# Kernel tuning notes

Measured on AMD Instinct MI355X. Metric: run time of the kernel, lower is better.

The kernel has to match this reference:

```python
import jax, jax.numpy as jnp
import numpy as np

N_REAL = 1_000_000
C_IN = 32
C_OUT = 32
PAD = 1_050_000


def setup_inputs() -> dict:
    key = jax.random.key(0)
    k_x, k_fn, k_w0, k_w1, k_w2, k_b = jax.random.split(key, 6)
    x = jax.random.normal(k_x, (N_REAL, C_IN), dtype=jnp.float32)
    face_neighborhood = jax.random.randint(k_fn, (N_REAL, 9), 0, PAD, dtype=jnp.int32)
    # real faces occupy the first N_REAL padded slots; the rest are pads
    face_is_pad = jnp.arange(PAD) >= N_REAL
    # kaiming-uniform-style init for [out, in] weights (fan_in = C_IN for 1x1 taps)
    bw = 1.0 / np.sqrt(C_IN)
    w0 = jax.random.uniform(k_w0, (C_OUT, C_IN), jnp.float32, -bw, bw)
    w1 = jax.random.uniform(k_w1, (C_OUT, C_IN), jnp.float32, -bw, bw)
    w2 = jax.random.uniform(k_w2, (C_OUT, C_IN), jnp.float32, -bw, bw)
    bb = 1.0 / np.sqrt(C_IN * 9)  # fan_in of the full (out,in,1,9) kernel
    bias = jax.random.uniform(k_b, (C_OUT,), jnp.float32, -bb, bb)
    return {"x": x, "w0": w0, "w1": w1, "w2": w2, "bias": bias,
            "face_neighborhood": face_neighborhood, "face_is_pad": face_is_pad,
            "pad_size": PAD}


def reference(x, w0, w1, w2, bias, face_neighborhood, face_is_pad, pad_size):
    # Scatter x into padded buffer: padded_x[~face_is_pad] = x (jit-safe via cumsum map)
    keep = jnp.logical_not(face_is_pad)
    src = jnp.cumsum(keep.astype(jnp.int32)) - 1  # index into x for each kept slot
    padded_x = jnp.where(keep[:, None], x[jnp.clip(src, 0, x.shape[0] - 1)],
                         jnp.zeros((), x.dtype))  # [pad_size, C]
    # Symmetric 1x9 filter = [w0, w1, w2, w1, w2, w1, w2, w1, w2]:
    # fold the 9 gathers into 3 groups before the tiny GEMMs.
    g0 = padded_x[face_neighborhood[:, 0]]
    g1 = (padded_x[face_neighborhood[:, 1]] + padded_x[face_neighborhood[:, 3]]
          + padded_x[face_neighborhood[:, 5]] + padded_x[face_neighborhood[:, 7]])
    g2 = (padded_x[face_neighborhood[:, 2]] + padded_x[face_neighborhood[:, 4]]
          + padded_x[face_neighborhood[:, 6]] + padded_x[face_neighborhood[:, 8]])
    out = (jnp.einsum('nc,oc->no', g0, w0)
           + jnp.einsum('nc,oc->no', g1, w1)
           + jnp.einsum('nc,oc->no', g2, w2)
           + bias)
    return out
```

## Files before the change

### kernel.cpp

```cpp
#include <hip/hip_runtime.h>
#include <hip/hip_fp16.h>

typedef _Float16 half8 __attribute__((ext_vector_type(8)));
typedef _Float16 half4v __attribute__((ext_vector_type(4)));
typedef float float4v __attribute__((ext_vector_type(4)));

#define BLOCK 256
#define ROWS_PER_BLOCK 64
#define ROWPITCH 104

__device__ _Float16 g_wh[6 * 512];

__global__ void prep_weights(const float* __restrict__ w0,
                             const float* __restrict__ w1,
                             const float* __restrict__ w2) {
    const int t = threadIdx.x;
    const int st = t >> 6;
    const int lane = t & 63;
    const int s = st >> 1, tt = st & 1;
    const float* w = (s == 0) ? w0 : (s == 1) ? w1 : w2;
    const int o = tt * 16 + (lane & 15);
    const int k = (lane >> 4) * 8;
    #pragma unroll
    for (int j = 0; j < 8; ++j)
        g_wh[st * 512 + lane * 8 + j] = (_Float16)w[o * 32 + k + j];
}

__global__ __launch_bounds__(BLOCK) void face_conv_kernel(
    const float* __restrict__ x,
    const float* __restrict__ bias,
    const int* __restrict__ fn,
    float* __restrict__ out,
    int N)
{
    __shared__ _Float16 A[4][16 * ROWPITCH];

    const int tid  = threadIdx.x;
    const int wave = tid >> 6;
    const int lane = tid & 63;
    const int m16  = lane & 15;
    const int quad = lane >> 4;
    const int oct  = lane >> 3;
    const int m8   = lane & 7;

    half8 bfrag[3][2];
    #pragma unroll
    for (int s = 0; s < 3; ++s)
        #pragma unroll
        for (int t = 0; t < 2; ++t)
            bfrag[s][t] = *(const half8*)(g_wh + (s * 2 + t) * 512 + lane * 8);
    const float bias0 = bias[m16];
    const float bias1 = bias[16 + m16];

    const int base = blockIdx.x * ROWS_PER_BLOCK + wave * 16;
    _Float16* Aw = A[wave];

    int idx[2][9];
    #pragma unroll
    for (int it = 0; it < 2; ++it) {
        int r = base + it * 8 + oct;
        r = (r < N) ? r : (N - 1);
        const int* fr = fn + (long)r * 9;
        #pragma unroll
        for (int j = 0; j < 9; ++j) idx[it][j] = __builtin_nontemporal_load(fr + j);
    }

    #pragma unroll
    for (int it = 0; it < 2; ++it) {
        float4v v[9];
        #pragma unroll
        for (int j = 0; j < 9; ++j) {
            const int id = idx[it][j];
            if ((unsigned)id < (unsigned)N) {
                v[j] = *(const float4v*)(x + (long)id * 32 + m8 * 4);
            } else {
                v[j] = (float4v){0.f, 0.f, 0.f, 0.f};
            }
        }
        const float4v g0 = v[0];
        const float4v g1 = v[1] + v[3] + v[5] + v[7];
        const float4v g2 = v[2] + v[4] + v[6] + v[8];
        _Float16* dst = Aw + (it * 8 + oct) * ROWPITCH + m8 * 4;
        *(half4v*)(dst)      = (half4v){(_Float16)g0.x, (_Float16)g0.y, (_Float16)g0.z, (_Float16)g0.w};
        *(half4v*)(dst + 32) = (half4v){(_Float16)g1.x, (_Float16)g1.y, (_Float16)g1.z, (_Float16)g1.w};
        *(half4v*)(dst + 64) = (half4v){(_Float16)g2.x, (_Float16)g2.y, (_Float16)g2.z, (_Float16)g2.w};
    }

    __syncthreads();

    float4v acc0 = {0.f, 0.f, 0.f, 0.f}, acc1 = {0.f, 0.f, 0.f, 0.f};
    #pragma unroll
    for (int s = 0; s < 3; ++s) {
        half8 a = *(half8*)(Aw + m16 * ROWPITCH + s * 32 + quad * 8);
        acc0 = __builtin_amdgcn_mfma_f32_16x16x32_f16(a, bfrag[s][0], acc0, 0, 0, 0);
        acc1 = __builtin_amdgcn_mfma_f32_16x16x32_f16(a, bfrag[s][1], acc1, 0, 0, 0);
    }

    #pragma unroll
    for (int i = 0; i < 4; ++i) {
        const int r = base + quad * 4 + i;
        if (r < N) {
            __builtin_nontemporal_store(acc0[i] + bias0, &out[(long)r * 32 + m16]);
            __builtin_nontemporal_store(acc1[i] + bias1, &out[(long)r * 32 + 16 + m16]);
        }
    }
}

extern "C" void kernel_launch(void* const* d_in, const int* in_sizes, int n_in,
                              void* d_out, int out_size, void* d_ws, size_t ws_size,
                              hipStream_t stream) {
    const float* x    = (const float*)d_in[0];
    const float* w0   = (const float*)d_in[1];
    const float* w1   = (const float*)d_in[2];
    const float* w2   = (const float*)d_in[3];
    const float* bias = (const float*)d_in[4];
    const int*   fn   = (const int*)d_in[5];
    float* out = (float*)d_out;

    const int N = in_sizes[0] / 32;
    const int blocks = (N + ROWS_PER_BLOCK - 1) / ROWS_PER_BLOCK;

    prep_weights<<<1, 384, 0, stream>>>(w0, w1, w2);
    face_conv_kernel<<<blocks, BLOCK, 0, stream>>>(x, bias, fn, out, N);
}
```

Baseline: 378.4 us.

## Pre-convert x to fp16 in workspace and gather half-precision rows

Adds a pass that converts x to fp16 into the workspace buffer. A new conv kernel then gathers 16-byte half8 chunks, so each random gather moves half the bytes, and neighbor indices are loaded as int4 vectors. The cost is an extra streaming read of x plus a write of the fp16 copy. The values are also rounded to fp16 before the group sums, where before they were summed in fp32 first. The fp32 path remains as a fallback when the workspace is too small.

After: 401.6 us. +6.1%, slower.

```diff
diff --git a/kernel.cpp b/kernel.cpp
--- a/kernel.cpp
+++ b/kernel.cpp
@@ -4,6 +4,7 @@
 typedef _Float16 half8 __attribute__((ext_vector_type(8)));
 typedef _Float16 half4v __attribute__((ext_vector_type(4)));
 typedef float float4v __attribute__((ext_vector_type(4)));
+typedef int int4a __attribute__((ext_vector_type(4), aligned(4)));
 
 #define BLOCK 256
 #define ROWS_PER_BLOCK 64
@@ -26,6 +27,97 @@
         g_wh[st * 512 + lane * 8 + j] = (_Float16)w[o * 32 + k + j];
 }
 
+__global__ __launch_bounds__(256) void convert_x(const float* __restrict__ x,
+                                                 _Float16* __restrict__ xh,
+                                                 int n8) {
+    const int stride = gridDim.x * 256;
+    for (int i = blockIdx.x * 256 + threadIdx.x; i < n8; i += stride) {
+        const float4v a = __builtin_nontemporal_load(reinterpret_cast<const float4v*>(x) + 2 * (long)i);
+        const float4v b = __builtin_nontemporal_load(reinterpret_cast<const float4v*>(x) + 2 * (long)i + 1);
+        half8 h = {(_Float16)a.x, (_Float16)a.y, (_Float16)a.z, (_Float16)a.w,
+                   (_Float16)b.x, (_Float16)b.y, (_Float16)b.z, (_Float16)b.w};
+        *(half8*)(xh + 8 * (long)i) = h;
+    }
+}
+
+__global__ __launch_bounds__(BLOCK) void face_conv_f16(
+    const _Float16* __restrict__ xh,
+    const float* __restrict__ bias,
+    const int* __restrict__ fn,
+    float* __restrict__ out,
+    int N)
+{
+    __shared__ alignas(16) _Float16 A[4][16 * ROWPITCH];
+
+    const int tid  = threadIdx.x;
+    const int wave = tid >> 6;
+    const int lane = tid & 63;
+    const int m16  = lane & 15;
+    const int quad = lane >> 4;
+    const int r    = lane >> 2;
+    const int c8   = (lane & 3) * 8;
+
+    half8 bfrag[3][2];
+    #pragma unroll
+    for (int s = 0; s < 3; ++s)
+        #pragma unroll
+        for (int t = 0; t < 2; ++t)
+            bfrag[s][t] = *(const half8*)(g_wh + (s * 2 + t) * 512 + lane * 8);
+    const float bias0 = bias[m16];
+    const float bias1 = bias[16 + m16];
+
+    const int base = blockIdx.x * ROWS_PER_BLOCK + wave * 16;
+    _Float16* Aw = A[wave];
+
+    int row = base + r;
+    row = (row < N) ? row : (N - 1);
+    const int* fr = fn + (long)row * 9;
+    const int4a i03 = __builtin_nontemporal_load(reinterpret_cast<const int4a*>(fr));
+    const int4a i47 = __builtin_nontemporal_load(reinterpret_cast<const int4a*>(fr + 4));
+    const int  i8s  = __builtin_nontemporal_load(fr + 8);
+    const int idx[9] = {i03.x, i03.y, i03.z, i03.w, i47.x, i47.y, i47.z, i47.w, i8s};
+
+    half8 v[9];
+    #pragma unroll
+    for (int j = 0; j < 9; ++j) {
+        const int id = idx[j];
+        if ((unsigned)id < (unsigned)N) {
+            v[j] = *(const half8*)(xh + (long)id * 32 + c8);
+        } else {
+            v[j] = (half8){0, 0, 0, 0, 0, 0, 0, 0};
+        }
+    }
+    half8 g0 = v[0], g1, g2;
+    #pragma unroll
+    for (int e = 0; e < 8; ++e) {
+        g1[e] = (_Float16)((float)v[1][e] + (float)v[3][e] + (float)v[5][e] + (float)v[7][e]);
+        g2[e] = (_Float16)((float)v[2][e] + (float)v[4][e] + (float)v[6][e] + (float)v[8][e]);
+    }
+    _Float16* dst = Aw + r * ROWPITCH + c8;
+    *(half8*)(dst)      = g0;
+    *(half8*)(dst + 32) = g1;
+    *(half8*)(dst + 64) = g2;
+
+    __syncthreads();
+
+    float4v acc0 = {0.f, 0.f, 0.f, 0.f}, acc1 = {0.f, 0.f, 0.f, 0.f};
+    #pragma unroll
+    for (int s = 0; s < 3; ++s) {
+        half8 a = *(half8*)(Aw + m16 * ROWPITCH + s * 32 + quad * 8);
+        acc0 = __builtin_amdgcn_mfma_f32_16x16x32_f16(a, bfrag[s][0], acc0, 0, 0, 0);
+        acc1 = __builtin_amdgcn_mfma_f32_16x16x32_f16(a, bfrag[s][1], acc1, 0, 0, 0);
+    }
+
+    #pragma unroll
+    for (int i = 0; i < 4; ++i) {
+        const int rr = base + quad * 4 + i;
+        if (rr < N) {
+            __builtin_nontemporal_store(acc0[i] + bias0, &out[(long)rr * 32 + m16]);
+            __builtin_nontemporal_store(acc1[i] + bias1, &out[(long)rr * 32 + 16 + m16]);
+        }
+    }
+}
+
 __global__ __launch_bounds__(BLOCK) void face_conv_kernel(
     const float* __restrict__ x,
     const float* __restrict__ bias,
@@ -33,7 +125,7 @@
     float* __restrict__ out,
     int N)
 {
-    __shared__ _Float16 A[4][16 * ROWPITCH];
+    __shared__ alignas(16) _Float16 A[4][16 * ROWPITCH];
 
     const int tid  = threadIdx.x;
     const int wave = tid >> 6;
@@ -121,5 +213,14 @@
     const int blocks = (N + ROWS_PER_BLOCK - 1) / ROWS_PER_BLOCK;
 
     prep_weights<<<1, 384, 0, stream>>>(w0, w1, w2);
-    face_conv_kernel<<<blocks, BLOCK, 0, stream>>>(x, bias, fn, out, N);
-}
+
+    const size_t need = (size_t)N * 32 * sizeof(_Float16);
+    if (d_ws != nullptr && ws_size >= need) {
+        _Float16* xh = (_Float16*)d_ws;
+        const int n8 = N * 4;
+        convert_x<<<2048, 256, 0, stream>>>(x, xh, n8);
+        face_conv_f16<<<blocks, BLOCK, 0, stream>>>(xh, bias, fn, out, N);
+    } else {
+        face_conv_kernel<<<blocks, BLOCK, 0, stream>>>(x, bias, fn, out, N);
+    }
+}
```

## Issue all 18 gather loads upfront with 4 lanes per row and vectorized index loads

Applied to the files above, without the earlier changes.

Each lane now owns a quarter-row (8 floats), so every row is gathered by 4 lanes, and all 18 float4 gathers are issued at once with branchless clamped addresses. Invalid indices are zeroed afterwards with selects. Index loads become two int4 loads plus one scalar, and the LDS store becomes a single half8 per group. A sched_barrier keeps the loads grouped, a min-waves hint is added to launch_bounds, and the goal is more memory-level parallelism in the random gather at the cost of higher register pressure.

Measured after the change: 374.8 us. About the same (-1.0%).

```diff
diff --git a/kernel.cpp b/kernel.cpp
--- a/kernel.cpp
+++ b/kernel.cpp
@@ -4,6 +4,7 @@
 typedef _Float16 half8 __attribute__((ext_vector_type(8)));
 typedef _Float16 half4v __attribute__((ext_vector_type(4)));
 typedef float float4v __attribute__((ext_vector_type(4)));
+typedef int int4a __attribute__((ext_vector_type(4), aligned(4)));
 
 #define BLOCK 256
 #define ROWS_PER_BLOCK 64
@@ -26,22 +27,47 @@
         g_wh[st * 512 + lane * 8 + j] = (_Float16)w[o * 32 + k + j];
 }
 
-__global__ __launch_bounds__(BLOCK) void face_conv_kernel(
+__global__ __launch_bounds__(BLOCK, 4) void face_conv_kernel(
     const float* __restrict__ x,
     const float* __restrict__ bias,
     const int* __restrict__ fn,
     float* __restrict__ out,
     int N)
 {
-    __shared__ _Float16 A[4][16 * ROWPITCH];
+    __shared__ alignas(16) _Float16 A[4][16 * ROWPITCH];
 
     const int tid  = threadIdx.x;
     const int wave = tid >> 6;
     const int lane = tid & 63;
     const int m16  = lane & 15;
     const int quad = lane >> 4;
-    const int oct  = lane >> 3;
-    const int m8   = lane & 7;
+    const int r    = lane >> 2;
+    const int c4   = lane & 3;
+
+    const int base = blockIdx.x * ROWS_PER_BLOCK + wave * 16;
+    _Float16* Aw = A[wave];
+
+    int row = base + r;
+    row = (row < N) ? row : (N - 1);
+    const int* fr = fn + (long)row * 9;
+    const int4a i03 = __builtin_nontemporal_load(reinterpret_cast<const int4a*>(fr));
+    const int4a i47 = __builtin_nontemporal_load(reinterpret_cast<const int4a*>(fr + 4));
+    const int  i8s  = __builtin_nontemporal_load(fr + 8);
+    const int idx[9] = {i03.x, i03.y, i03.z, i03.w, i47.x, i47.y, i47.z, i47.w, i8s};
+
+    const float* p[9];
+    #pragma unroll
+    for (int j = 0; j < 9; ++j) {
+        const unsigned id = (unsigned)idx[j];
+        const int cl = (id < (unsigned)N) ? (int)id : 0;
+        p[j] = x + (long)cl * 32 + c4 * 8;
+    }
+
+    float4v vA[9], vB[9];
+    #pragma unroll
+    for (int j = 0; j < 9; ++j) vA[j] = *(const float4v*)(p[j]);
+    #pragma unroll
+    for (int j = 0; j < 9; ++j) vB[j] = *(const float4v*)(p[j] + 4);
 
     half8 bfrag[3][2];
     #pragma unroll
@@ -52,56 +78,47 @@
     const float bias0 = bias[m16];
     const float bias1 = bias[16 + m16];
 
-    const int base = blockIdx.x * ROWS_PER_BLOCK + wave * 16;
-    _Float16* Aw = A[wave];
+    __builtin_amdgcn_sched_barrier(0);
 
-    int idx[2][9];
+    const float4v z = {0.f, 0.f, 0.f, 0.f};
+    float4v a[9], b[9];
     #pragma unroll
-    for (int it = 0; it < 2; ++it) {
-        int r = base + it * 8 + oct;
-        r = (r < N) ? r : (N - 1);
-        const int* fr = fn + (long)r * 9;
-        #pragma unroll
-        for (int j = 0; j < 9; ++j) idx[it][j] = __builtin_nontemporal_load(fr + j);
+    for (int j = 0; j < 9; ++j) {
+        const bool ok = (unsigned)idx[j] < (unsigned)N;
+        a[j] = ok ? vA[j] : z;
+        b[j] = ok ? vB[j] : z;
     }
+    const float4v g0a = a[0];
+    const float4v g0b = b[0];
+    const float4v g1a = a[1] + a[3] + a[5] + a[7];
+    const float4v g1b = b[1] + b[3] + b[5] + b[7];
+    const float4v g2a = a[2] + a[4] + a[6] + a[8];
+    const float4v g2b = b[2] + b[4] + b[6] + b[8];
 
-    #pragma unroll
-    for (int it = 0; it < 2; ++it) {
-        float4v v[9];
-        #pragma unroll
-        for (int j = 0; j < 9; ++j) {
-            const int id = idx[it][j];
-            if ((unsigned)id < (unsigned)N) {
-                v[j] = *(const float4v*)(x + (long)id * 32 + m8 * 4);
-            } else {
-                v[j] = (float4v){0.f, 0.f, 0.f, 0.f};
-            }
-        }
-        const float4v g0 = v[0];
-        const float4v g1 = v[1] + v[3] + v[5] + v[7];
-        const float4v g2 = v[2] + v[4] + v[6] + v[8];
-        _Float16* dst = Aw + (it * 8 + oct) * ROWPITCH + m8 * 4;
-        *(half4v*)(dst)      = (half4v){(_Float16)g0.x, (_Float16)g0.y, (_Float16)g0.z, (_Float16)g0.w};
-        *(half4v*)(dst + 32) = (half4v){(_Float16)g1.x, (_Float16)g1.y, (_Float16)g1.z, (_Float16)g1.w};
-        *(half4v*)(dst + 64) = (half4v){(_Float16)g2.x, (_Float16)g2.y, (_Float16)g2.z, (_Float16)g2.w};
-    }
+    _Float16* dst = Aw + r * ROWPITCH + c4 * 8;
+    *(half8*)(dst) = (half8){(_Float16)g0a.x, (_Float16)g0a.y, (_Float16)g0a.z, (_Float16)g0a.w,
+                             (_Float16)g0b.x, (_Float16)g0b.y, (_Float16)g0b.z, (_Float16)g0b.w};
+    *(half8*)(dst + 32) = (half8){(_Float16)g1a.x, (_Float16)g1a.y, (_Float16)g1a.z, (_Float16)g1a.w,
+                                  (_Float16)g1b.x, (_Float16)g1b.y, (_Float16)g1b.z, (_Float16)g1b.w};
+    *(half8*)(dst + 64) = (half8){(_Float16)g2a.x, (_Float16)g2a.y, (_Float16)g2a.z, (_Float16)g2a.w,
+                                  (_Float16)g2b.x, (_Float16)g2b.y, (_Float16)g2b.z, (_Float16)g2b.w};
 
     __syncthreads();
 
     float4v acc0 = {0.f, 0.f, 0.f, 0.f}, acc1 = {0.f, 0.f, 0.f, 0.f};
     #pragma unroll
     for (int s = 0; s < 3; ++s) {
-        half8 a = *(half8*)(Aw + m16 * ROWPITCH + s * 32 + quad * 8);
-        acc0 = __builtin_amdgcn_mfma_f32_16x16x32_f16(a, bfrag[s][0], acc0, 0, 0, 0);
-        acc1 = __builtin_amdgcn_mfma_f32_16x16x32_f16(a, bfrag[s][1], acc1, 0, 0, 0);
+        half8 av = *(half8*)(Aw + m16 * ROWPITCH + s * 32 + quad * 8);
+        acc0 = __builtin_amdgcn_mfma_f32_16x16x32_f16(av, bfrag[s][0], acc0, 0, 0, 0);
+        acc1 = __builtin_amdgcn_mfma_f32_16x16x32_f16(av, bfrag[s][1], acc1, 0, 0, 0);
     }
 
     #pragma unroll
     for (int i = 0; i < 4; ++i) {
-        const int r = base + quad * 4 + i;
-        if (r < N) {
-            __builtin_nontemporal_store(acc0[i] + bias0, &out[(long)r * 32 + m16]);
-            __builtin_nontemporal_store(acc1[i] + bias1, &out[(long)r * 32 + 16 + m16]);
+        const int rr = base + quad * 4 + i;
+        if (rr < N) {
+            __builtin_nontemporal_store(acc0[i] + bias0, &out[(long)rr * 32 + m16]);
+            __builtin_nontemporal_store(acc1[i] + bias1, &out[(long)rr * 32 + 16 + m16]);
         }
     }
 }
```
